# Optimization experiments

Measured on AMD Instinct MI355X. Metric: run time of the kernel, lower is better.

## Reference

```python
import jax, jax.numpy as jnp
import numpy as np

N_QUBITS = 4

def _rx(theta):
    # RX(t) = [[cos t/2, -i sin t/2], [-i sin t/2, cos t/2]]; theta scalar or [B]
    c = jnp.cos(theta / 2).astype(jnp.complex64)
    s = (-1j * jnp.sin(theta / 2)).astype(jnp.complex64)
    return jnp.stack([jnp.stack([c, s], -1), jnp.stack([s, c], -1)], -2)

def _ry(theta):
    c = jnp.cos(theta / 2).astype(jnp.complex64)
    s = jnp.sin(theta / 2).astype(jnp.complex64)
    return jnp.stack([jnp.stack([c, -s], -1), jnp.stack([s, c], -1)], -2)

def _rz(theta):
    e0 = jnp.exp(-0.5j * theta).astype(jnp.complex64)
    e1 = jnp.exp(0.5j * theta).astype(jnp.complex64)
    z = jnp.zeros_like(e0)
    return jnp.stack([jnp.stack([e0, z], -1), jnp.stack([z, e1], -1)], -2)

def _apply_1q(psi, U, wire):
    # psi: [B,2,2,2,2]; U: [2,2] (shared) or [B,2,2] (per-batch angle)
    psi = jnp.moveaxis(psi, 1 + wire, -1)
    if U.ndim == 3:
        psi = jnp.einsum('bij,b...j->b...i', U, psi)
    else:
        psi = jnp.einsum('ij,b...j->b...i', U, psi)
    return jnp.moveaxis(psi, -1, 1 + wire)

def _cnot(psi, c, t):
    psi = jnp.moveaxis(psi, (1 + c, 1 + t), (-2, -1))
    psi = jnp.concatenate([psi[..., 0:1, :], psi[..., 1:2, ::-1]], axis=-2)
    return jnp.moveaxis(psi, (-2, -1), (1 + c, 1 + t))

def _measure_all_z(psi):
    p = psi.real ** 2 + psi.imag ** 2  # [B,2,2,2,2]
    outs = []
    for w in range(N_QUBITS):
        shape = [1] * (N_QUBITS + 1)
        shape[1 + w] = 2
        z = jnp.array([1.0, -1.0], dtype=p.dtype).reshape(shape)
        outs.append(jnp.sum(p * z, axis=tuple(range(1, N_QUBITS + 1))))
    return jnp.stack(outs, -1)  # [B,4]

def _qlayer(x, theta):
    # x: [B,4] encoding angles; theta: [4] trainable RX angles
    B = x.shape[0]
    psi = jnp.zeros((B, 2 ** N_QUBITS), jnp.complex64).at[:, 0].set(1.0)
    psi = psi.reshape((B,) + (2,) * N_QUBITS)
    # encoder: rx(w0), ry(w1), rz(w2), rx(w3)
    psi = _apply_1q(psi, _rx(x[:, 0]), 0)
    psi = _apply_1q(psi, _ry(x[:, 1]), 1)
    psi = _apply_1q(psi, _rz(x[:, 2]), 2)
    psi = _apply_1q(psi, _rx(x[:, 3]), 3)
    # trainable RX on each wire
    for w in range(N_QUBITS):
        psi = _apply_1q(psi, _rx(theta[w]), w)
    # CNOT ring 0->1,1->2,2->3,3->0
    for w in range(N_QUBITS):
        psi = _cnot(psi, w, (w + 1) % N_QUBITS)
    return _measure_all_z(psi)

def setup_inputs() -> dict:
    key = jax.random.key(0)
    ks = jax.random.split(key, 13)
    T, B, D, H, Q = 128, 2048, 128, 4, 4
    s = 1.0 / np.sqrt(D + H)
    inp = {
        'inputs': jax.random.normal(ks[0], (T, B, D), jnp.float32),
        'Wf': jax.random.uniform(ks[1], (Q, D + H), jnp.float32, -s, s),
        'bf': jax.random.uniform(ks[2], (Q,), jnp.float32, -s, s),
        'Wi': jax.random.uniform(ks[3], (Q, D + H), jnp.float32, -s, s),
        'bi': jax.random.uniform(ks[4], (Q,), jnp.float32, -s, s),
        'Wu': jax.random.uniform(ks[5], (Q, D + H), jnp.float32, -s, s),
        'bu': jax.random.uniform(ks[6], (Q,), jnp.float32, -s, s),
        'Wo': jax.random.uniform(ks[7], (Q, D + H), jnp.float32, -s, s),
        'bo': jax.random.uniform(ks[8], (Q,), jnp.float32, -s, s),
        'theta_f': jax.random.uniform(ks[9], (Q,), jnp.float32, 0.0, 2 * np.pi),
        'theta_i': jax.random.uniform(ks[10], (Q,), jnp.float32, 0.0, 2 * np.pi),
        'theta_u': jax.random.uniform(ks[11], (Q,), jnp.float32, 0.0, 2 * np.pi),
        'theta_o': jax.random.uniform(ks[12], (Q,), jnp.float32, 0.0, 2 * np.pi),
    }
    return inp

def reference(inputs, Wf, bf, Wi, bi, Wu, bu, Wo, bo, theta_f, theta_i, theta_u, theta_o):
    T, B, D = inputs.shape
    H = N_QUBITS  # hidden_dim == n_qubits (required by elementwise gate math)
    h0 = jnp.zeros((B, H), inputs.dtype)
    c0 = jnp.zeros((B, H), inputs.dtype)

    def step(carry, x):
        hx, cx = carry
        comb = jnp.concatenate([x, hx], axis=1)  # [B, D+H]
        f = jax.nn.sigmoid(_qlayer(comb @ Wf.T + bf, theta_f))
        i = jax.nn.sigmoid(_qlayer(comb @ Wi.T + bi, theta_i))
        g = jnp.tanh(_qlayer(comb @ Wu.T + bu, theta_u))
        o = jax.nn.sigmoid(_qlayer(comb @ Wo.T + bo, theta_o))
        cx = f * cx + i * g
        hx = o * jnp.tanh(cx)
        return (hx, cx), hx

    (hx, cx), stacked = jax.lax.scan(step, (h0, c0), inputs)
    return stacked, hx, cx
```

## Files before the change

### kernel.cpp

```cpp
#include <hip/hip_runtime.h>
#include <stdint.h>

__device__ __forceinline__ float fast_exp(float x) {
  return __builtin_amdgcn_exp2f(x * 1.4426950408889634f);
}
__device__ __forceinline__ float fast_rcp(float x) {
  return __builtin_amdgcn_rcpf(x);
}
__device__ __forceinline__ float fast_cos(float x) {
  return __builtin_amdgcn_cosf(__builtin_amdgcn_fractf(x * 0.15915494309189535f));
}
__device__ __forceinline__ float fast_sigmoid(float x) {
  return fast_rcp(1.0f + fast_exp(-x));
}
__device__ __forceinline__ float fast_tanh(float x) {
  return 1.0f - 2.0f * fast_rcp(1.0f + fast_exp(2.0f * x));
}
__device__ __forceinline__ float sigmoid_poly(float x) {
  float x2 = x * x;
  float p = fmaf(fmaf(fmaf(-2.1085373e-4f, x2, 2.0833334e-3f), x2,
                      -2.0833334e-2f), x2, 0.25f);
  return fmaf(x, p, 0.5f);
}
__device__ __forceinline__ float tanh_pade(float x) {
  float x2 = x * x;
  float num = x * fmaf(x2 + 105.f, x2, 945.f);
  float den = fmaf(fmaf(15.f, x2, 420.f), x2, 945.f);
  return num * fast_rcp(den);
}

template <int CTRL>
__device__ __forceinline__ float dppf(float v) {
  return __int_as_float(__builtin_amdgcn_update_dpp(
      0, __float_as_int(v), CTRL, 0xf, 0xf, true));
}
#define QP_XOR1 0xB1
#define QP_XOR2 0x4E
#define QP_XOR3 0x1B

__device__ __forceinline__ void gload_lds16(const float* gp, const float* lp) {
  __builtin_amdgcn_global_load_lds(
      reinterpret_cast<const uint32_t __attribute__((address_space(1)))*>(
          reinterpret_cast<uintptr_t>(gp)),
      reinterpret_cast<uint32_t __attribute__((address_space(3)))*>(
          reinterpret_cast<uintptr_t>(lp)),
      16, 0, 0);
}

__global__ __launch_bounds__(64) void qlstm_gemm(
    const float* __restrict__ x,
    const float* __restrict__ Wf, const float* __restrict__ bf,
    const float* __restrict__ Wi, const float* __restrict__ bi,
    const float* __restrict__ Wu, const float* __restrict__ bu,
    const float* __restrict__ Wo, const float* __restrict__ bo,
    const float* __restrict__ thf, const float* __restrict__ thi,
    const float* __restrict__ thu, const float* __restrict__ tho,
    float* __restrict__ Z, long long rows, int B, int D)
{
  __shared__ float tile[64][36];
  const long long base = (long long)blockIdx.x * 64;
  const int tid = threadIdx.x;
  const long long r = base + tid;
  const bool valid = r < rows;
  const int ldw = D + 4;
  const float* Ws[4] = {Wf, Wi, Wu, Wo};
  const float* bs[4] = {bf, bi, bu, bo};
  const float* ts[4] = {thf, thi, thu, tho};

  float acc[12];
#pragma unroll
  for (int g = 0; g < 4; ++g) {
    acc[g * 3 + 0] = bs[g][0] + ts[g][0];
    acc[g * 3 + 1] = bs[g][1];
    acc[g * 3 + 2] = bs[g][3] + ts[g][3];
  }

  const int nkc = D >> 5;
  for (int kc = 0; kc < nkc; ++kc) {
#pragma unroll
    for (int i = 0; i < 8; ++i) {
      int f = i * 64 + tid;
      int row = f >> 3, col = (f & 7) * 4;
      long long gr = base + row;
      if (gr < rows) {
        float4 v = *(const float4*)(x + gr * (long long)D + kc * 32 + col);
        *(float4*)&tile[row][col] = v;
      }
    }
    __syncthreads();
    if (valid) {
#pragma unroll
      for (int k = 0; k < 32; k += 4) {
        float4 xv = *(float4*)&tile[tid][k];
#pragma unroll
        for (int g = 0; g < 4; ++g) {
#pragma unroll
          for (int jj = 0; jj < 3; ++jj) {
            int row2 = (jj == 2) ? 3 : jj;
            const float* wp = Ws[g] + row2 * ldw + kc * 32 + k;
            acc[g * 3 + jj] += xv.x * wp[0] + xv.y * wp[1] + xv.z * wp[2] + xv.w * wp[3];
          }
        }
      }
    }
    __syncthreads();
  }

  if (valid) {
    float* zp = Z + r * 16;
#pragma unroll
    for (int g = 0; g < 4; ++g) {
      *(float4*)(zp + g * 4) =
          make_float4(acc[g * 3 + 0], acc[g * 3 + 1], acc[g * 3 + 2], 0.f);
    }
  }
}

__global__ __launch_bounds__(64) void qlstm_scan4(
    const float* __restrict__ Z,
    const float* __restrict__ Wf, const float* __restrict__ Wi,
    const float* __restrict__ Wu, const float* __restrict__ Wo,
    const float* __restrict__ thf, const float* __restrict__ thi,
    const float* __restrict__ thu, const float* __restrict__ tho,
    float* __restrict__ out, int T, int B, int D)
{
  __shared__ float lds[2][16][256];
  const int tid = threadIdx.x;
  const int gid = blockIdx.x * 64 + tid;
  const int b = gid >> 2, q = gid & 3;
  if (b >= B) return;

  const float* Wg = (q == 0) ? Wf : (q == 1) ? Wi : (q == 2) ? Wu : Wo;
  const float* th = (q == 0) ? thf : (q == 1) ? thi : (q == 2) ? thu : tho;
  const int ldw = D + 4;
  const float ct1 = fast_cos(th[1]);
  const float m2c = fast_cos(th[2]);

  float wh[3][4];
#pragma unroll
  for (int jj = 0; jj < 3; ++jj) {
    int row = (jj == 2) ? 3 : jj;
#pragma unroll
    for (int d = 0; d < 4; ++d)
      wh[jj][d] = Wg[row * ldw + D + (q ^ d)];
  }
  const bool e0 = ((q & 1) == 0);
  const bool e1 = ((q & 2) == 0);

  float h = 0.f, c = 0.f;

  const float* Zlane = Z + (size_t)gid * 4;
  const size_t tstr = (size_t)16 * B;
  const size_t pstr = (size_t)4 * B;
  float* hx  = out + (size_t)T * B * 4;
  float* cxp = hx + (size_t)B * 4;

  auto step = [&](float4 zv, int t) {
    float z0 = zv.x, z1 = zv.y, z2 = zv.z;
    float h1 = dppf<QP_XOR1>(h);
    float h2 = dppf<QP_XOR2>(h);
    float h3 = dppf<QP_XOR3>(h);
    float a0 = fmaf(wh[0][0], h, fmaf(wh[0][1], h1, fmaf(wh[0][2], h2, fmaf(wh[0][3], h3, z0))));
    float a1 = fmaf(wh[1][0], h, fmaf(wh[1][1], h1, fmaf(wh[1][2], h2, fmaf(wh[1][3], h3, z1))));
    float a2 = fmaf(wh[2][0], h, fmaf(wh[2][1], h1, fmaf(wh[2][2], h2, fmaf(wh[2][3], h3, z2))));
    float m0 = fast_cos(a0);
    float m1 = ct1 * fast_cos(a1);
    float m3 = fast_cos(a2);
    float m01 = m0 * m1, m23 = m2c * m3;
    float g0 = m1 * m23;
    float g1 = m01;
    float g2 = m01 * m2c;
    float g3 = m01 * m23;
    float x0 = dppf<QP_XOR1>(g0);
    float x1 = dppf<QP_XOR1>(g1);
    float x2 = dppf<QP_XOR1>(g2);
    float x3 = dppf<QP_XOR1>(g3);
    float s0 = e0 ? g0 : x1;
    float s1 = e0 ? x0 : g1;
    float s2 = e0 ? g2 : x3;
    float s3 = e0 ? x2 : g3;
    float y0 = dppf<QP_XOR2>(s0);
    float y1 = dppf<QP_XOR2>(s1);
    float y2 = dppf<QP_XOR2>(s2);
    float y3 = dppf<QP_XOR2>(s3);
    float wf_ = e1 ? s0 : y2;
    float wi_ = e1 ? s1 : y3;
    float wu_ = e1 ? y0 : s2;
    float wo_ = e1 ? y1 : s3;
    float fg = sigmoid_poly(wf_);
    float ig = sigmoid_poly(wi_);
    float ug = tanh_pade(wu_);
    float og = sigmoid_poly(wo_);
    c = fmaf(fg, c, ig * ug);
    h = og * tanh_pade(c);
    out[(size_t)t * pstr + gid] = h;
  };

  auto issue_chunk = [&](int tbase, int buf) {
#pragma unroll
    for (int tl = 0; tl < 16; ++tl) {
      gload_lds16(Zlane + (size_t)(tbase + tl) * tstr, &lds[buf][tl][0]);
    }
  };

  if (T >= 32 && (T & 15) == 0) {
    const int nch = T >> 4;
    issue_chunk(0, 0);
    issue_chunk(16, 1);
    asm volatile("s_waitcnt vmcnt(16)" ::: "memory");
    __builtin_amdgcn_sched_barrier(0);
    int cur = 0;
    for (int k = 0; k < nch; ++k) {
      const int tb = k << 4;
#pragma unroll
      for (int tl = 0; tl < 16; ++tl) {
        float4 zv = *(const float4*)&lds[cur][tl][tid * 4];
        step(zv, tb + tl);
      }
      if (k + 2 < nch) issue_chunk((k + 2) << 4, cur);
      cur ^= 1;
      if (k + 1 < nch) {
        if (k + 2 < nch) {
          asm volatile("s_waitcnt vmcnt(32)" ::: "memory");
        } else {
          asm volatile("s_waitcnt vmcnt(16)" ::: "memory");
        }
        __builtin_amdgcn_sched_barrier(0);
      }
    }
  } else {
    for (int t = 0; t < T; ++t) {
      float4 zv = *(const float4*)(Zlane + (size_t)t * tstr);
      step(zv, t);
    }
  }

  hx[gid]  = h;
  cxp[gid] = c;
}

struct GK {
  float wh[4][3][4];
  float ct1[4];
  float m2c[4];
};

__device__ __forceinline__ void load_gk(GK& K,
    const float* Wf, const float* Wi, const float* Wu, const float* Wo,
    const float* thf, const float* thi, const float* thu, const float* tho,
    int D)
{
  const float* Ws[4] = {Wf, Wi, Wu, Wo};
  const float* ts[4] = {thf, thi, thu, tho};
  const int ldw = D + 4;
#pragma unroll
  for (int g = 0; g < 4; ++g) {
#pragma unroll
    for (int jj = 0; jj < 3; ++jj) {
      int row = (jj == 2) ? 3 : jj;
#pragma unroll
      for (int qq = 0; qq < 4; ++qq)
        K.wh[g][jj][qq] = Ws[g][row * ldw + D + qq];
    }
    K.ct1[g] = fast_cos(ts[g][1]);
    K.m2c[g] = fast_cos(ts[g][2]);
  }
}

__device__ __forceinline__ void qlstm_step_sc(const float a[12], const GK& K,
                                              float h[4], float c[4])
{
  float gv[4][4];
#pragma unroll
  for (int g = 0; g < 4; ++g) {
    float m0 = fast_cos(a[g * 3 + 0]);
    float m1 = K.ct1[g] * fast_cos(a[g * 3 + 1]);
    float m3 = fast_cos(a[g * 3 + 2]);
    float m01 = m0 * m1;
    float m23 = K.m2c[g] * m3;
    gv[g][0] = m1 * m23;
    gv[g][1] = m01;
    gv[g][2] = m01 * K.m2c[g];
    gv[g][3] = m01 * m23;
  }
#pragma unroll
  for (int qq = 0; qq < 4; ++qq) {
    float fg = fast_sigmoid(gv[0][qq]);
    float ig = fast_sigmoid(gv[1][qq]);
    float ug = fast_tanh(gv[2][qq]);
    float og = fast_sigmoid(gv[3][qq]);
    c[qq] = fg * c[qq] + ig * ug;
    h[qq] = og * fast_tanh(c[qq]);
  }
}

__global__ __launch_bounds__(256) void qlstm_fused(
    const float* __restrict__ x,
    const float* __restrict__ Wf, const float* __restrict__ bf,
    const float* __restrict__ Wi, const float* __restrict__ bi,
    const float* __restrict__ Wu, const float* __restrict__ bu,
    const float* __restrict__ Wo, const float* __restrict__ bo,
    const float* __restrict__ thf, const float* __restrict__ thi,
    const float* __restrict__ thu, const float* __restrict__ tho,
    float* __restrict__ out, int T, int B, int D)
{
  int b = blockIdx.x * 256 + threadIdx.x;
  if (b >= B) return;
  GK K;
  load_gk(K, Wf, Wi, Wu, Wo, thf, thi, thu, tho, D);
  const float* Ws[4] = {Wf, Wi, Wu, Wo};
  const float* bs[4] = {bf, bi, bu, bo};
  const float* ts[4] = {thf, thi, thu, tho};
  const int ldw = D + 4;

  float base[12];
#pragma unroll
  for (int g = 0; g < 4; ++g) {
    base[g * 3 + 0] = bs[g][0] + ts[g][0];
    base[g * 3 + 1] = bs[g][1];
    base[g * 3 + 2] = bs[g][3] + ts[g][3];
  }

  float h[4] = {0.f, 0.f, 0.f, 0.f};
  float c[4] = {0.f, 0.f, 0.f, 0.f};
  float* hx  = out + (size_t)T * B * 4;
  float* cxp = hx + (size_t)B * 4;

  for (int t = 0; t < T; ++t) {
    float a[12];
#pragma unroll
    for (int j = 0; j < 12; ++j) a[j] = base[j];
    const float* xp = x + ((size_t)t * B + b) * D;
    for (int k = 0; k < D; k += 4) {
      float4 xv = *(const float4*)(xp + k);
#pragma unroll
      for (int g = 0; g < 4; ++g) {
        const float* W = Ws[g];
#pragma unroll
        for (int jj = 0; jj < 3; ++jj) {
          int row = (jj == 2) ? 3 : jj;
          const float* wp = W + row * ldw + k;
          a[g * 3 + jj] += xv.x * wp[0] + xv.y * wp[1] + xv.z * wp[2] + xv.w * wp[3];
        }
      }
    }
#pragma unroll
    for (int g = 0; g < 4; ++g) {
#pragma unroll
      for (int jj = 0; jj < 3; ++jj) {
        a[g * 3 + jj] += K.wh[g][jj][0] * h[0] + K.wh[g][jj][1] * h[1]
                       + K.wh[g][jj][2] * h[2] + K.wh[g][jj][3] * h[3];
      }
    }
    qlstm_step_sc(a, K, h, c);
    *(float4*)(out + ((size_t)t * B + b) * 4) = make_float4(h[0], h[1], h[2], h[3]);
  }
  *(float4*)(hx + (size_t)b * 4)  = make_float4(h[0], h[1], h[2], h[3]);
  *(float4*)(cxp + (size_t)b * 4) = make_float4(c[0], c[1], c[2], c[3]);
}

extern "C" void kernel_launch(void* const* d_in, const int* in_sizes, int n_in,
                              void* d_out, int out_size, void* d_ws, size_t ws_size,
                              hipStream_t stream)
{
  const float* x   = (const float*)d_in[0];
  const float* Wf  = (const float*)d_in[1];
  const float* bf  = (const float*)d_in[2];
  const float* Wi  = (const float*)d_in[3];
  const float* bi  = (const float*)d_in[4];
  const float* Wu  = (const float*)d_in[5];
  const float* bu  = (const float*)d_in[6];
  const float* Wo  = (const float*)d_in[7];
  const float* bo  = (const float*)d_in[8];
  const float* thf = (const float*)d_in[9];
  const float* thi = (const float*)d_in[10];
  const float* thu = (const float*)d_in[11];
  const float* tho = (const float*)d_in[12];

  int DH = in_sizes[1] / 4;
  int D  = DH - 4;
  long long TB = (long long)in_sizes[0] / D;
  int B = (int)(((long long)out_size - 4 * TB) / 8);
  int T = (int)(TB / B);

  size_t zbytes = (size_t)TB * 16 * sizeof(float);
  if (ws_size >= zbytes && (D & 31) == 0 && (B & 15) == 0) {
    float* Z = (float*)d_ws;
    int gblocks = (int)((TB + 63) / 64);
    qlstm_gemm<<<gblocks, 64, 0, stream>>>(x, Wf, bf, Wi, bi, Wu, bu, Wo, bo,
                                           thf, thi, thu, tho, Z, TB, B, D);
    int sthreads = B * 4;
    qlstm_scan4<<<(sthreads + 63) / 64, 64, 0, stream>>>(Z, Wf, Wi, Wu, Wo,
                                                         thf, thi, thu, tho,
                                                         (float*)d_out, T, B, D);
  } else {
    qlstm_fused<<<(B + 255) / 256, 256, 0, stream>>>(x, Wf, bf, Wi, bi, Wu, bu, Wo, bo,
                                                     thf, thi, thu, tho,
                                                     (float*)d_out, T, B, D);
  }
}
```

Baseline: 71.61 us.

## Warp-specialize GEMM kernel with producer wave and double-buffered LDS tiles

Splits the projection GEMM block into two waves. One wave loads x tiles from global memory into registers and stages them into a double-buffered LDS tile, while the other wave computes the dot products. This overlaps global loads with compute instead of serialising load, sync and compute per chunk. It doubles threads per block while only one wave computes, and it restricts the fast path to TB divisible by 64. The code also assumes nkc is at least 2.

```diff
diff --git a/kernel.cpp b/kernel.cpp
--- a/kernel.cpp
+++ b/kernel.cpp
@@ -47,7 +47,7 @@
       16, 0, 0);
 }
 
-__global__ __launch_bounds__(64) void qlstm_gemm(
+__global__ __launch_bounds__(128) void qlstm_gemm(
     const float* __restrict__ x,
     const float* __restrict__ Wf, const float* __restrict__ bf,
     const float* __restrict__ Wi, const float* __restrict__ bi,
@@ -57,12 +57,14 @@
     const float* __restrict__ thu, const float* __restrict__ tho,
     float* __restrict__ Z, long long rows, int B, int D)
 {
-  __shared__ float tile[64][36];
+  __shared__ float tile[2][64][36];
   const long long base = (long long)blockIdx.x * 64;
-  const int tid = threadIdx.x;
-  const long long r = base + tid;
-  const bool valid = r < rows;
+  const int tid  = threadIdx.x;
+  const int wave = tid >> 6;
+  const int lane = tid & 63;
   const int ldw = D + 4;
+  const int nkc = D >> 5;
+
   const float* Ws[4] = {Wf, Wi, Wu, Wo};
   const float* bs[4] = {bf, bi, bu, bo};
   const float* ts[4] = {thf, thi, thu, tho};
@@ -75,38 +77,73 @@
     acc[g * 3 + 2] = bs[g][3] + ts[g][3];
   }
 
-  const int nkc = D >> 5;
-  for (int kc = 0; kc < nkc; ++kc) {
+  float4 A[8];
+
+  if (wave == 0) {
 #pragma unroll
     for (int i = 0; i < 8; ++i) {
-      int f = i * 64 + tid;
+      int f = i * 64 + lane;
       int row = f >> 3, col = (f & 7) * 4;
-      long long gr = base + row;
-      if (gr < rows) {
-        float4 v = *(const float4*)(x + gr * (long long)D + kc * 32 + col);
-        *(float4*)&tile[row][col] = v;
-      }
-    }
-    __syncthreads();
-    if (valid) {
+      A[i] = *(const float4*)(x + (base + row) * (long long)D + 0 * 32 + col);
+    }
+    asm volatile("s_waitcnt vmcnt(0)" ::: "memory");
+#pragma unroll
+    for (int i = 0; i < 8; ++i) {
+      int f = i * 64 + lane;
+      int row = f >> 3, col = (f & 7) * 4;
+      *(float4*)&tile[0][row][col] = A[i];
+    }
+#pragma unroll
+    for (int i = 0; i < 8; ++i) {
+      int f = i * 64 + lane;
+      int row = f >> 3, col = (f & 7) * 4;
+      A[i] = *(const float4*)(x + (base + row) * (long long)D + 1 * 32 + col);
+    }
+  }
+  __syncthreads();
+
+  for (int m = 0; m < nkc; ++m) {
+    if (wave == 0) {
+      if (m + 1 < nkc) {
+        asm volatile("s_waitcnt vmcnt(0)" ::: "memory");
+        const int bufi = (m + 1) & 1;
+#pragma unroll
+        for (int i = 0; i < 8; ++i) {
+          int f = i * 64 + lane;
+          int row = f >> 3, col = (f & 7) * 4;
+          *(float4*)&tile[bufi][row][col] = A[i];
+        }
+        if (m + 2 < nkc) {
+#pragma unroll
+          for (int i = 0; i < 8; ++i) {
+            int f = i * 64 + lane;
+            int row = f >> 3, col = (f & 7) * 4;
+            A[i] = *(const float4*)(x + (base + row) * (long long)D +
+                                    (m + 2) * 32 + col);
+          }
+        }
+      }
+    } else {
+      const float(*tb)[36] = tile[m & 1];
 #pragma unroll
       for (int k = 0; k < 32; k += 4) {
-        float4 xv = *(float4*)&tile[tid][k];
+        float4 xv = *(const float4*)&tb[lane][k];
 #pragma unroll
         for (int g = 0; g < 4; ++g) {
 #pragma unroll
           for (int jj = 0; jj < 3; ++jj) {
             int row2 = (jj == 2) ? 3 : jj;
-            const float* wp = Ws[g] + row2 * ldw + kc * 32 + k;
+            const float* wp = Ws[g] + row2 * ldw + m * 32 + k;
             acc[g * 3 + jj] += xv.x * wp[0] + xv.y * wp[1] + xv.z * wp[2] + xv.w * wp[3];
           }
         }
       }
     }
-    __syncthreads();
-  }
-
-  if (valid) {
+    if (m + 1 < nkc) __syncthreads();
+  }
+
+  if (wave == 1) {
+    const long long r = base + lane;
     float* zp = Z + r * 16;
 #pragma unroll
     for (int g = 0; g < 4; ++g) {
@@ -384,11 +421,11 @@
   int T = (int)(TB / B);
 
   size_t zbytes = (size_t)TB * 16 * sizeof(float);
-  if (ws_size >= zbytes && (D & 31) == 0 && (B & 15) == 0) {
+  if (ws_size >= zbytes && (D & 31) == 0 && (B & 15) == 0 && (TB & 63) == 0) {
     float* Z = (float*)d_ws;
-    int gblocks = (int)((TB + 63) / 64);
-    qlstm_gemm<<<gblocks, 64, 0, stream>>>(x, Wf, bf, Wi, bi, Wu, bu, Wo, bo,
-                                           thf, thi, thu, tho, Z, TB, B, D);
+    int gblocks = (int)(TB / 64);
+    qlstm_gemm<<<gblocks, 128, 0, stream>>>(x, Wf, bf, Wi, bi, Wu, bu, Wo, bo,
+                                            thf, thi, thu, tho, Z, TB, B, D);
     int sthreads = B * 4;
     qlstm_scan4<<<(sthreads + 63) / 64, 64, 0, stream>>>(Z, Wf, Wi, Wu, Wo,
                                                          thf, thi, thu, tho,
```

After: 121.4 us. 1.7x slower.
